# Kernel optimization log

Measured on AMD Instinct MI355X. Metric: run time of the kernel, lower is better.

## Reference

```python
import jax, jax.numpy as jnp
import numpy as np
import math

Z, N = 4, 128
EMB, L0, MLPH, GEO = 16, 32, 64, 64
NB, NH = 32, 128
C = MLPH + GEO
BETA, MAXR = 5.0, 10.0
Y0 = 0.5 / math.sqrt(math.pi)  # spherical harmonic l=0


def setup_inputs() -> dict:
    key = jax.random.key(0)
    ks = jax.random.split(key, 24)
    g = lambda i, s: jax.random.normal(ks[i], s, jnp.float32)
    inp = {}
    inp['features'] = jax.random.randint(ks[0], (Z, N, 1), 0, 6)
    inp['geometry'] = g(1, (Z, N, 3))
    inp['mask'] = jnp.ones((Z, N), jnp.float32)
    emb = g(2, (6, EMB))
    inp['emb'] = emb.at[5].set(0.0)  # padding_idx=5
    # radial MLP weights per conv layer (basis->h->h->mul_out*mul_in)
    inp['r0w0'] = g(3, (NB, NH)); inp['r0w1'] = g(4, (NH, NH)); inp['r0w2'] = g(5, (NH, L0 * EMB))
    inp['r1w0'] = g(6, (NB, NH)); inp['r1w1'] = g(7, (NH, NH)); inp['r1w2'] = g(8, (NH, L0 * L0))
    inp['r2w0'] = g(9, (NB, NH)); inp['r2w1'] = g(10, (NH, NH)); inp['r2w2'] = g(11, (NH, MLPH * L0))
    # ResnetPointnet (3 -> GEO per atom, two residual FC blocks)
    inp['pn_w0'] = g(12, (3, GEO)) * 0.3; inp['pn_b0'] = jnp.zeros((GEO,), jnp.float32)
    inp['pn_w1a'] = g(13, (GEO, GEO)) * 0.1; inp['pn_b1a'] = jnp.zeros((GEO,), jnp.float32)
    inp['pn_w1b'] = g(14, (GEO, GEO)) * 0.1; inp['pn_b1b'] = jnp.zeros((GEO,), jnp.float32)
    inp['pn_w2a'] = g(15, (GEO, GEO)) * 0.1; inp['pn_b2a'] = jnp.zeros((GEO,), jnp.float32)
    inp['pn_w2b'] = g(16, (GEO, GEO)) * 0.1; inp['pn_b2b'] = jnp.zeros((GEO,), jnp.float32)
    # output MLP + per-atom BatchNorm1d(natoms) params
    inp['e1_w'] = g(17, (C, C)) * 0.05; inp['e1_b'] = jnp.zeros((C,), jnp.float32)
    inp['bn1_g'] = jnp.ones((N,), jnp.float32); inp['bn1_b'] = jnp.zeros((N,), jnp.float32)
    inp['e2_w'] = g(18, (C, 2 * C)) * 0.05; inp['e2_b'] = jnp.zeros((2 * C,), jnp.float32)
    inp['bn2_g'] = jnp.ones((N,), jnp.float32); inp['bn2_b'] = jnp.zeros((N,), jnp.float32)
    return inp


def _sp(x):
    return jax.nn.softplus(BETA * x) / BETA


def _ssp(x):
    return _sp(x) - math.log(2.0) / BETA


def _leaky(x):
    return jnp.where(x > 0, x, 0.2 * x)


def _radial(radii, w0, w1, w2):
    # CosineBasisModel: smooth cosine^2 bumps then small MLP (e3nn-style /sqrt(fan_in))
    centers = jnp.linspace(0.0, MAXR, NB)
    step = centers[1] - centers[0]
    x = (radii[..., None] - centers) / step
    basis = jnp.where(jnp.abs(x) < 1.0, jnp.cos(0.5 * jnp.pi * x) ** 2, 0.0)  # [z,a,b,NB]
    h = _ssp(basis @ w0 / math.sqrt(NB))
    h = _ssp(h @ w1 / math.sqrt(NH))
    return h @ w2 / math.sqrt(NH)  # [z,a,b,dout*din]


def _bn(x, gamma, beta):
    # torch BatchNorm1d(natoms) on [Z, natoms, C]: normalize over (Z, C) per atom slot
    mu = jnp.mean(x, axis=(0, 2), keepdims=True)
    var = jnp.var(x, axis=(0, 2), keepdims=True)
    xn = (x - mu) * jax.lax.rsqrt(var + 1e-5)
    return xn * gamma[None, :, None] + beta[None, :, None]


def reference(features, geometry, mask, emb,
              r0w0, r0w1, r0w2, r1w0, r1w1, r1w2, r2w0, r2w1, r2w2,
              pn_w0, pn_b0, pn_w1a, pn_b1a, pn_w1b, pn_b1b,
              pn_w2a, pn_b2a, pn_w2b, pn_b2b,
              e1_w, e1_b, bn1_g, bn1_b, e2_w, e2_b, bn2_g, bn2_b):
    # constants(): pairwise geometry, detached in the original
    diff = jax.lax.stop_gradient(geometry[:, None, :, :] - geometry[:, :, None, :])  # [z,a,b,3]
    radii = jnp.linalg.norm(diff, axis=-1)  # [z,a,b]

    # ResnetPointnet: per-atom geometric features
    net = geometry @ pn_w0 + pn_b0
    for (wa, ba, wb, bb) in ((pn_w1a, pn_b1a, pn_w1b, pn_b1b), (pn_w2a, pn_b2a, pn_w2b, pn_b2b)):
        dx = jax.nn.relu(net) @ wa + ba
        dx = jax.nn.relu(dx) @ wb + bb
        net = net + dx
    geo_pn = net * mask[..., None]  # [z,n,GEO]

    # embedding
    f = emb[features[..., 0]]  # [z,n,EMB]

    # equivariant kernel-conv layers; all reps are l=0 so Y = Y0 constant
    dims = ((EMB, L0, r0w0, r0w1, r0w2), (L0, L0, r1w0, r1w1, r1w2), (L0, MLPH, r2w0, r2w1, r2w2))
    for (din, dout, w0, w1, w2) in dims:
        f = f / math.sqrt(N)
        K = _radial(radii, w0, w1, w2).reshape(Z, N, N, dout, din)
        f = jnp.einsum('zabij,zbj,zb->zai', K, f, mask) * Y0
        f = _sp(f)               # GatedBlock with all-scalar Rs -> scalar act only
        f = f * mask[..., None]

    feat = jnp.concatenate([f, geo_pn], axis=2)  # [z,n,C]
    x = _leaky(_bn(feat @ e1_w + e1_b, bn1_g, bn1_b))
    x = _leaky(_bn(x @ e2_w + e2_b, bn2_g, bn2_b))
    out = jnp.sum(x * mask[..., None], axis=1)  # Aggregate(axis=1, sum)
    return out  # [Z, 2*C]
```

## Files before the change

### kernel.cpp

```cpp
#include <hip/hip_runtime.h>
#include <math.h>

#define Zc   4
#define Nc   128
#define EMBc 16
#define L0c  32
#define MLPHc 64
#define GEOc 64
#define NBc  32
#define NHc  128
#define Cc   128
#define SLc  64

typedef float  f32x4  __attribute__((ext_vector_type(4)));
typedef short  bf16x8 __attribute__((ext_vector_type(8)));

union FragU {
    bf16x8 v;
    unsigned short u[8];
    uint2 q2[2];
};

struct P {
    const float *geom, *mask, *emb;
    const int*   features;
    const float *pw0,*pb0,*w1a,*b1a,*w1b,*b1b,*w2a,*b2a,*w2b,*b2b;
    const float *r00,*r01,*r02, *r10,*r11,*r12, *r20,*r21,*r22;
    const float *e1w,*e1b,*bn1g,*bn1b,*e2w,*e2b,*bn2g,*bn2b;
    unsigned short *h2buf, *gt, *packs;
    float *part, *f0, *geo_pn, *outp;
};

__device__ __forceinline__ float sp5(float x){
    float y = 5.0f * x;
    float t = fabsf(y);
    return (fmaxf(y, 0.0f) + log1pf(__expf(-t))) * 0.2f;
}
__device__ __forceinline__ float ssp5_post(float y){
    float e = __expf(-fabsf(y));
    float u = fmaxf(y, 0.0f) + __logf(1.0f + e);
    return fmaf(0.2f, u, -0.13862943611198906f);
}
__device__ __forceinline__ unsigned int cvtpk_bf16(float a, float b){
    unsigned int r;
    asm("v_cvt_pk_bf16_f32 %0, %1, %2" : "=v"(r) : "v"(a), "v"(b));
    return r;
}
__device__ __forceinline__ unsigned short f2bf(float f){
    unsigned int u = __float_as_uint(f);
    unsigned int r = (u + 0x7FFFu + ((u >> 16) & 1u)) >> 16;
    return (unsigned short)r;
}
__device__ __forceinline__ int kmap(int l, int e){
    return 4*((l >> 4) & 3) + (e & 3) + 16*(e >> 2);
}

__device__ void init_dev(int bx, const P& p, char* smem)
{
    float* cur = (float*)smem;
    float* tmp = cur + 4*GEOc;
    int t = threadIdx.x;
    if (bx < 128){
        int g  = t >> 6;
        int c  = t & 63;
        int zn = bx*4 + g;
        float gx = p.geom[zn*3+0], gy = p.geom[zn*3+1], gz = p.geom[zn*3+2];
        float v = fmaf(gx, p.pw0[0*GEOc+c], fmaf(gy, p.pw0[1*GEOc+c],
                  fmaf(gz, p.pw0[2*GEOc+c], p.pb0[c])));
        const float* WA[2] = {p.w1a, p.w2a}; const float* BA[2] = {p.b1a, p.b2a};
        const float* WB[2] = {p.w1b, p.w2b}; const float* BB[2] = {p.b1b, p.b2b};
        #pragma unroll
        for (int blk = 0; blk < 2; blk++){
            cur[g*GEOc + c] = v;
            __syncthreads();
            float s = BA[blk][c];
            for (int k = 0; k < GEOc; k++)
                s = fmaf(fmaxf(cur[g*GEOc + k], 0.0f), WA[blk][k*GEOc+c], s);
            tmp[g*GEOc + c] = s;
            __syncthreads();
            float s2 = BB[blk][c];
            for (int k = 0; k < GEOc; k++)
                s2 = fmaf(fmaxf(tmp[g*GEOc + k], 0.0f), WB[blk][k*GEOc+c], s2);
            v = v + s2;
            __syncthreads();
        }
        p.geo_pn[zn*GEOc + c] = v * p.mask[zn];
        if (c < EMBc){
            int fi = p.features[zn];
            p.f0[zn*EMBc + c] = p.emb[fi*EMBc + c] * p.mask[zn] * 0.0022038655607334227f;
        }
    } else if (bx < 368){
        int j = bx - 128;
        int layer = j / 80;
        int sub = j % 80;
        const float* w0s = (layer == 0) ? p.r00 : (layer == 1) ? p.r10 : p.r20;
        const float* w1s = (layer == 0) ? p.r01 : (layer == 1) ? p.r11 : p.r21;
        unsigned short* p0 = p.packs + layer*4096;
        unsigned short* p1 = p.packs + 12288 + layer*16384;
        int idx = sub*256 + t;
        if (idx < 4096){
            int t8 = idx >> 9, l = (idx >> 3) & 63, e = idx & 7;
            int k = kmap(l, e);
            int n = (t8 << 4) + (l & 15);
            p0[idx] = f2bf(w0s[k*NHc + n] * 0.8838834764831844f);
        } else {
            int jj = idx - 4096;
            int fid = jj >> 9, l = (jj >> 3) & 63, e = jj & 7;
            int kk = fid >> 3, t8 = fid & 7;
            int k = 32*kk + kmap(l, e);
            int n = 16*t8 + (l & 15);
            p1[jj] = f2bf(w1s[k*NHc + n] * 0.4419417382415922f);
        }
    } else {
        for (int i = t; i < Zc*2*Cc; i += 256) p.outp[i] = 0.0f;
    }
}

__device__ void pairmlp_dev(int vb, const P& p, char* smem)
{
    char* lb = smem;
    int t   = threadIdx.x;
    int w   = t >> 6;
    int l   = t & 63;
    int g16 = l >> 4;
    int c   = l & 15;
    int layer = vb >> 10;
    int p0  = (vb & 1023) * 64;
    int z   = p0 >> 14;
    int a   = (p0 >> 7) & 127;
    int b0  = p0 & 127;

    if (b0 + 16*w + 15 < a) return;

    const unsigned short* wp0 = p.packs + layer*4096;
    const unsigned short* wp1 = p.packs + 12288 + layer*16384;
    unsigned short* h2 = p.h2buf + (size_t)layer * ((size_t)Zc*Nc*Nc*NHc);

    int bp = b0 + 16*w + c;
    float ax = p.geom[(z*Nc + a)*3 + 0];
    float ay = p.geom[(z*Nc + a)*3 + 1];
    float az = p.geom[(z*Nc + a)*3 + 2];
    float dx = p.geom[(z*Nc + bp)*3 + 0] - ax;
    float dy = p.geom[(z*Nc + bp)*3 + 1] - ay;
    float dz = p.geom[(z*Nc + bp)*3 + 2] - az;
    float rm = sqrtf(dx*dx + dy*dy + dz*dz);

    FragU af;
    #pragma unroll
    for (int e = 0; e < 8; e++){
        int k = kmap(l, e);
        float x = fmaf(rm, 3.1f, -(float)k);
        float v = 0.0f;
        if (fabsf(x) < 1.0f){ float cc = __cosf(1.57079632679f*x); v = cc*cc; }
        af.u[e] = (unsigned short)cvtpk_bf16(v, v);
    }

    f32x4 acc[8];
    #pragma unroll
    for (int t8 = 0; t8 < 8; t8++) acc[t8] = (f32x4){0.f,0.f,0.f,0.f};
    #pragma unroll
    for (int t8 = 0; t8 < 8; t8++){
        bf16x8 bf = *reinterpret_cast<const bf16x8*>(wp0 + ((t8*64 + l) << 3));
        acc[t8] = __builtin_amdgcn_mfma_f32_16x16x32_bf16(af.v, bf, acc[t8], 0, 0, 0);
    }
    #pragma unroll
    for (int t8 = 0; t8 < 8; t8++){
        #pragma unroll
        for (int rg = 0; rg < 4; rg++){
            int m = 16*w + 4*g16 + rg;
            int n = 16*t8 + c;
            int off = ((m << 8) + (n << 1)) ^ ((m & 7) << 4);
            *(unsigned short*)(lb + off) = (unsigned short)cvtpk_bf16(ssp5_post(acc[t8][rg]), 0.0f);
        }
    }

    f32x4 acc2[8];
    #pragma unroll
    for (int t8 = 0; t8 < 8; t8++) acc2[t8] = (f32x4){0.f,0.f,0.f,0.f};
    int mrow = 16*w + c;
    int sw   = (mrow & 7) << 4;
    #pragma unroll
    for (int kk = 0; kk < 4; kk++){
        int ob = (mrow << 8) + (kk << 6) + (g16 << 3);
        FragU a2;
        a2.q2[0] = *(const uint2*)(lb + (ob ^ sw));
        a2.q2[1] = *(const uint2*)(lb + ((ob + 32) ^ sw));
        #pragma unroll
        for (int t8 = 0; t8 < 8; t8++){
            bf16x8 bf = *reinterpret_cast<const bf16x8*>(wp1 + (((kk*8 + t8)*64 + l) << 3));
            acc2[t8] = __builtin_amdgcn_mfma_f32_16x16x32_bf16(a2.v, bf, acc2[t8], 0, 0, 0);
        }
    }
    size_t zbase = (size_t)z*Nc*Nc*NHc;
    #pragma unroll
    for (int t8 = 0; t8 < 8; t8++){
        #pragma unroll
        for (int rg = 0; rg < 4; rg++){
            int m = 16*w + 4*g16 + rg;
            int b = b0 + m;
            unsigned short val = (unsigned short)cvtpk_bf16(ssp5_post(acc2[t8][rg]), 0.0f);
            h2[zbase + ((size_t)a*Nc + b)*NHc + 16*t8 + c] = val;
        }
    }
}

template<int DIN, int DOUT>
__device__ void gmat_dev(int vb, const float* f, const float* w2,
                         unsigned short* gt, char* smem)
{
    float (*fsh)[DIN] = (float (*)[DIN])smem;
    int t  = threadIdx.x;
    int bx = vb & 63, by = vb >> 6;
    int zb0 = bx * 8;
    if (t < 8*DIN){
        int r = t / DIN, j = t % DIN;
        fsh[r][j] = f[(zb0 + r)*DIN + j];
    }
    __syncthreads();
    int mi = by * 256 + t;
    int m_ = mi & (NHc-1);
    int i_ = mi >> 7;
    const float* wrow = w2 + (size_t)(m_*DOUT + i_) * DIN;
    float s[8];
    #pragma unroll
    for (int r = 0; r < 8; r++) s[r] = 0.0f;
    #pragma unroll
    for (int j4 = 0; j4 < DIN/4; j4++){
        float4 wv4 = *reinterpret_cast<const float4*>(&wrow[j4*4]);
        #pragma unroll
        for (int q = 0; q < 4; q++){
            float wv = reinterpret_cast<const float*>(&wv4)[q];
            int j = j4*4 + q;
            #pragma unroll
            for (int r = 0; r < 8; r++)
                s[r] = fmaf(fsh[r][j], wv, s[r]);
        }
    }
    int z = zb0 >> 7;
    #pragma unroll
    for (int r = 0; r < 8; r++){
        int b = (zb0 + r) & (Nc-1);
        gt[((size_t)z*DOUT + i_)*(Nc*NHc) + b*NHc + m_] = (unsigned short)cvtpk_bf16(s[r], s[r]);
    }
}

template<int DIN, int DOUT>
__device__ void egmat_dev(int vb, const float* part, const float* mask,
                          const float* w2, unsigned short* gt, char* smem)
{
    float (*fsh)[DIN] = (float (*)[DIN])smem;
    int t  = threadIdx.x;
    int bx = vb & 63, by = vb >> 6;
    int zb0 = bx * 8;
    for (int idx = t; idx < 8*DIN; idx += 256){
        int r = idx / DIN, j = idx % DIN;
        int zb = zb0 + r;
        float s = 0.0f;
        #pragma unroll
        for (int sl = 0; sl < SLc; sl++)
            s += part[(size_t)sl*(Zc*Nc*DIN) + zb*DIN + j];
        float m = mask[zb];
        fsh[r][j] = sp5(s) * m * m * 0.0022038655607334227f;
    }
    __syncthreads();
    int mi = by * 256 + t;
    int m_ = mi & (NHc-1);
    int i_ = mi >> 7;
    const float* wrow = w2 + (size_t)(m_*DOUT + i_) * DIN;
    float s[8];
    #pragma unroll
    for (int r = 0; r < 8; r++) s[r] = 0.0f;
    #pragma unroll
    for (int j4 = 0; j4 < DIN/4; j4++){
        float4 wv4 = *reinterpret_cast<const float4*>(&wrow[j4*4]);
        #pragma unroll
        for (int q = 0; q < 4; q++){
            float wv = reinterpret_cast<const float*>(&wv4)[q];
            int j = j4*4 + q;
            #pragma unroll
            for (int r = 0; r < 8; r++)
                s[r] = fmaf(fsh[r][j], wv, s[r]);
        }
    }
    int z = zb0 >> 7;
    #pragma unroll
    for (int r = 0; r < 8; r++){
        int b = (zb0 + r) & (Nc-1);
        gt[((size_t)z*DOUT + i_)*(Nc*NHc) + b*NHc + m_] = (unsigned short)cvtpk_bf16(s[r], s[r]);
    }
}

template<int DOUT, int KS>
__device__ void gemm3_dev(int vb, const unsigned short* h2, const unsigned short* gt,
                          float* partial, char* smem)
{
    constexpr int NS   = (Nc*NHc)/KS;
    constexpr int ROWB = KS*2;
    unsigned short* Ash = (unsigned short*)smem;
    unsigned short* Bsh = (unsigned short*)(smem + 64*ROWB);
    int t = threadIdx.x;
    int w = t >> 6, l = t & 63;
    int g16 = l >> 4, c16 = l & 15;
    int s  = vb % NS;
    int at = (vb / NS) & 1;
    int z  = vb / (NS*2);
    int a0 = at*64;
    int k0 = s*KS;

    {
        constexpr int ITA = (64*(KS/8))/256;
        #pragma unroll
        for (int it = 0; it < ITA; it++){
            int idx = it*256 + t;
            int r = idx / (KS/8), c8 = idx % (KS/8);
            int aRow = a0 + r;
            int kk = k0 + c8*8;
            int b  = kk >> 7;
            int m8 = kk & (NHc-1);
            const unsigned short* srcp = (b >= aRow)
                ? h2 + ((size_t)(z*Nc + aRow))*(Nc*NHc) + b*NHc + m8
                : h2 + ((size_t)(z*Nc + b))*(Nc*NHc) + aRow*NHc + m8;
            uint4 v = *reinterpret_cast<const uint4*>(srcp);
            int byte = (r*ROWB + c8*16) ^ ((r & 7) << 4);
            *reinterpret_cast<uint4*>((char*)Ash + byte) = v;
        }
    }
    {
        const unsigned short* src = gt + ((size_t)z*DOUT)*(Nc*NHc) + k0;
        constexpr int ITB = (DOUT*(KS/8))/256;
        #pragma unroll
        for (int it = 0; it < ITB; it++){
            int idx = it*256 + t;
            int r = idx / (KS/8), c8 = idx % (KS/8);
            uint4 v = *reinterpret_cast<const uint4*>(src + (size_t)r*(Nc*NHc) + c8*8);
            int byte = (r*ROWB + c8*16) ^ ((r & 7) << 4);
            *reinterpret_cast<uint4*>((char*)Bsh + byte) = v;
        }
    }
    __syncthreads();

    constexpr int NT = DOUT/16;
    f32x4 acc[NT];
    #pragma unroll
    for (int nt = 0; nt < NT; nt++) acc[nt] = (f32x4){0.f,0.f,0.f,0.f};
    int ar  = 16*w + c16;
    int asw = (ar & 7) << 4;
    #pragma unroll
    for (int ks = 0; ks < KS/32; ks++){
        FragU afr;
        int abyte = ar*ROWB + ks*64 + g16*8;
        afr.q2[0] = *(const uint2*)((char*)Ash + (abyte ^ asw));
        afr.q2[1] = *(const uint2*)((char*)Ash + ((abyte + 32) ^ asw));
        #pragma unroll
        for (int nt = 0; nt < NT; nt++){
            int br  = nt*16 + c16;
            int bsw = (br & 7) << 4;
            int bbyte = br*ROWB + ks*64 + g16*8;
            FragU bfr;
            bfr.q2[0] = *(const uint2*)((char*)Bsh + (bbyte ^ bsw));
            bfr.q2[1] = *(const uint2*)((char*)Bsh + ((bbyte + 32) ^ bsw));
            acc[nt] = __builtin_amdgcn_mfma_f32_16x16x32_bf16(afr.v, bfr.v, acc[nt], 0, 0, 0);
        }
    }
    #pragma unroll
    for (int nt = 0; nt < NT; nt++){
        #pragma unroll
        for (int rg = 0; rg < 4; rg++){
            int a = a0 + 16*w + 4*g16 + rg;
            int i = nt*16 + c16;
            partial[(((size_t)s*Zc + z)*Nc + a)*DOUT + i] = acc[nt][rg];
        }
    }
}

__device__ void tail_dev(int n, const P& p, char* smem)
{
    float* feat = (float*)smem;
    float* xln  = feat + Zc*Cc;
    float* r1   = xln + Zc*Cc;
    float* r2   = r1 + 4;
    int t = threadIdx.x;

    {
        int z = t >> 6, i = t & 63;
        float s = 0.0f;
        #pragma unroll
        for (int sl = 0; sl < SLc; sl++)
            s += p.part[((size_t)sl*Zc*Nc + z*Nc + n)*MLPHc + i];
        float m = p.mask[z*Nc + n];
        feat[z*Cc + i] = sp5(s) * m;
        feat[z*Cc + MLPHc + i] = p.geo_pn[(z*Nc + n)*GEOc + i];
    }
    __syncthreads();

    int c  = t & 127;
    int zh = t >> 7;
    float x1v[2];
    float sum = 0.0f, sq = 0.0f;
    #pragma unroll
    for (int q = 0; q < 2; q++){
        int z = zh*2 + q;
        float s = p.e1b[c];
        for (int k = 0; k < Cc; k++) s = fmaf(feat[z*Cc + k], p.e1w[k*Cc + c], s);
        x1v[q] = s; sum += s; sq = fmaf(s, s, sq);
    }
    #pragma unroll
    for (int off = 32; off > 0; off >>= 1){
        sum += __shfl_down(sum, off);
        sq  += __shfl_down(sq,  off);
    }
    if ((t & 63) == 0){ r1[t >> 6] = sum; r2[t >> 6] = sq; }
    __syncthreads();
    {
        float tot  = r1[0]+r1[1]+r1[2]+r1[3];
        float totq = r2[0]+r2[1]+r2[2]+r2[3];
        float mu   = tot * (1.0f/512.0f);
        float var  = totq * (1.0f/512.0f) - mu*mu;
        float rstd = rsqrtf(var + 1e-5f);
        float ga = p.bn1g[n], be = p.bn1b[n];
        #pragma unroll
        for (int q = 0; q < 2; q++){
            float v = (x1v[q] - mu) * rstd * ga + be;
            xln[(zh*2 + q)*Cc + c] = v > 0.0f ? v : 0.2f*v;
        }
    }
    __syncthreads();

    float x2v[4];
    sum = 0.0f; sq = 0.0f;
    #pragma unroll
    for (int z = 0; z < Zc; z++){
        float s = p.e2b[t];
        for (int k = 0; k < Cc; k++) s = fmaf(xln[z*Cc + k], p.e2w[k*2*Cc + t], s);
        x2v[z] = s; sum += s; sq = fmaf(s, s, sq);
    }
    #pragma unroll
    for (int off = 32; off > 0; off >>= 1){
        sum += __shfl_down(sum, off);
        sq  += __shfl_down(sq,  off);
    }
    if ((t & 63) == 0){ r1[t >> 6] = sum; r2[t >> 6] = sq; }
    __syncthreads();
    {
        float tot  = r1[0]+r1[1]+r1[2]+r1[3];
        float totq = r2[0]+r2[1]+r2[2]+r2[3];
        float mu   = tot * (1.0f/1024.0f);
        float var  = totq * (1.0f/1024.0f) - mu*mu;
        float rstd = rsqrtf(var + 1e-5f);
        float ga = p.bn2g[n], be = p.bn2b[n];
        #pragma unroll
        for (int z = 0; z < Zc; z++){
            float v = (x2v[z] - mu) * rstd * ga + be;
            v = v > 0.0f ? v : 0.2f*v;
            atomicAdd(&p.outp[z*2*Cc + t], v * p.mask[z*Nc + n]);
        }
    }
}

__global__ __launch_bounds__(256) void k_init_g(P p){
    __shared__ __align__(16) char smem[2048];
    init_dev(blockIdx.x, p, smem);
}
__global__ __launch_bounds__(256, 2) void k_pg(P p){
    __shared__ __align__(16) char smem[16384];
    int bx = blockIdx.x;
    if (bx < 3072){
        pairmlp_dev(bx, p, smem);
    } else {
        gmat_dev<16,32>(bx - 3072, p.f0, p.r02, p.gt, smem);
    }
}
template<int DIN, int DOUT>
__global__ __launch_bounds__(256) void k_egmat_g(P p, const float* w2){
    __shared__ __align__(16) char smem[8*DIN*4];
    egmat_dev<DIN,DOUT>(blockIdx.y*64 + blockIdx.x, p.part, p.mask, w2, p.gt, smem);
}
template<int DOUT, int KS>
__global__ __launch_bounds__(256) void k_gemm3_g(P p, const unsigned short* h2){
    __shared__ __align__(16) char smem[(64+DOUT)*KS*2];
    constexpr int NS = (Nc*NHc)/KS;
    int vb = (blockIdx.z*2 + blockIdx.y)*NS + blockIdx.x;
    gemm3_dev<DOUT,KS>(vb, h2, p.gt, p.part, smem);
}
__global__ __launch_bounds__(256) void k_tail_g(P p){
    __shared__ __align__(16) char smem[4224];
    tail_dev(blockIdx.x, p, smem);
}

extern "C" void kernel_launch(void* const* d_in, const int* in_sizes, int n_in,
                              void* d_out, int out_size, void* d_ws, size_t ws_size,
                              hipStream_t stream)
{
    P p;
    p.features = (const int*)  d_in[0];
    p.geom     = (const float*)d_in[1];
    p.mask     = (const float*)d_in[2];
    p.emb      = (const float*)d_in[3];
    p.r00 = (const float*)d_in[4];  p.r01 = (const float*)d_in[5];  p.r02 = (const float*)d_in[6];
    p.r10 = (const float*)d_in[7];  p.r11 = (const float*)d_in[8];  p.r12 = (const float*)d_in[9];
    p.r20 = (const float*)d_in[10]; p.r21 = (const float*)d_in[11]; p.r22 = (const float*)d_in[12];
    p.pw0 = (const float*)d_in[13]; p.pb0 = (const float*)d_in[14];
    p.w1a = (const float*)d_in[15]; p.b1a = (const float*)d_in[16];
    p.w1b = (const float*)d_in[17]; p.b1b = (const float*)d_in[18];
    p.w2a = (const float*)d_in[19]; p.b2a = (const float*)d_in[20];
    p.w2b = (const float*)d_in[21]; p.b2b = (const float*)d_in[22];
    p.e1w = (const float*)d_in[23]; p.e1b = (const float*)d_in[24];
    p.bn1g= (const float*)d_in[25]; p.bn1b= (const float*)d_in[26];
    p.e2w = (const float*)d_in[27]; p.e2b = (const float*)d_in[28];
    p.bn2g= (const float*)d_in[29]; p.bn2b= (const float*)d_in[30];

    float* ws = (float*)d_ws;
    p.h2buf = (unsigned short*)ws;
    p.gt    = (unsigned short*)(ws + 12582912);
    p.part  = ws + 12582912 + 2097152;
    p.f0    = p.part + 2097152;
    p.geo_pn= p.f0 + 8192;
    p.packs = (unsigned short*)(p.geo_pn + 32768);
    p.outp  = (float*)d_out;
    (void)ws_size; (void)in_sizes; (void)n_in; (void)out_size;

    const size_t H2L = (size_t)Zc*Nc*Nc*NHc;

    k_init_g<<<369, 256, 0, stream>>>(p);
    k_pg<<<4096, 256, 0, stream>>>(p);
    k_gemm3_g<32,256><<<dim3(64, 2, Zc), 256, 0, stream>>>(p, p.h2buf);
    k_egmat_g<32,32><<<dim3(64, 16), 256, 0, stream>>>(p, p.r12);
    k_gemm3_g<32,256><<<dim3(64, 2, Zc), 256, 0, stream>>>(p, p.h2buf + H2L);
    k_egmat_g<32,64><<<dim3(64, 32), 256, 0, stream>>>(p, p.r22);
    k_gemm3_g<64,256><<<dim3(64, 2, Zc), 256, 0, stream>>>(p, p.h2buf + 2*H2L);
    k_tail_g<<<128, 256, 0, stream>>>(p);
}
```

Measured before the change: 154.4 us.

## Split pair MLP into single-wave blocks over only needed triangular tiles

The fused pair-MLP/gmat kernel now launches 64-thread blocks, one wavefront per 16-pair tile, in place of 256-thread blocks holding four waves. Block indices map directly onto the triangular set of (a, b-chunk) tiles that are actually needed, so no launched waves exit early when their tile lies below the diagonal. The gmat part is re-tiled for 64 threads. This removes idle or early-exit waves and the load imbalance inside blocks. In exchange it launches more blocks, adds a sqrt-based index decode per block, and gives up the 2-blocks-per-CU launch bound.

```diff
diff --git a/kernel.cpp b/kernel.cpp
--- a/kernel.cpp
+++ b/kernel.cpp
@@ -116,27 +116,18 @@
     }
 }
 
-__device__ void pairmlp_dev(int vb, const P& p, char* smem)
+__device__ void pairmlp_dev(int layer, int z, int a, int bc, const P& p, char* smem)
 {
     char* lb = smem;
-    int t   = threadIdx.x;
-    int w   = t >> 6;
-    int l   = t & 63;
+    int l   = threadIdx.x;
     int g16 = l >> 4;
     int c   = l & 15;
-    int layer = vb >> 10;
-    int p0  = (vb & 1023) * 64;
-    int z   = p0 >> 14;
-    int a   = (p0 >> 7) & 127;
-    int b0  = p0 & 127;
-
-    if (b0 + 16*w + 15 < a) return;
 
     const unsigned short* wp0 = p.packs + layer*4096;
     const unsigned short* wp1 = p.packs + 12288 + layer*16384;
     unsigned short* h2 = p.h2buf + (size_t)layer * ((size_t)Zc*Nc*Nc*NHc);
 
-    int bp = b0 + 16*w + c;
+    int bp = bc + c;
     float ax = p.geom[(z*Nc + a)*3 + 0];
     float ay = p.geom[(z*Nc + a)*3 + 1];
     float az = p.geom[(z*Nc + a)*3 + 2];
@@ -167,17 +158,18 @@
     for (int t8 = 0; t8 < 8; t8++){
         #pragma unroll
         for (int rg = 0; rg < 4; rg++){
-            int m = 16*w + 4*g16 + rg;
+            int m = 4*g16 + rg;
             int n = 16*t8 + c;
             int off = ((m << 8) + (n << 1)) ^ ((m & 7) << 4);
             *(unsigned short*)(lb + off) = (unsigned short)cvtpk_bf16(ssp5_post(acc[t8][rg]), 0.0f);
         }
     }
+    __syncthreads();
 
     f32x4 acc2[8];
     #pragma unroll
     for (int t8 = 0; t8 < 8; t8++) acc2[t8] = (f32x4){0.f,0.f,0.f,0.f};
-    int mrow = 16*w + c;
+    int mrow = c;
     int sw   = (mrow & 7) << 4;
     #pragma unroll
     for (int kk = 0; kk < 4; kk++){
@@ -196,36 +188,40 @@
     for (int t8 = 0; t8 < 8; t8++){
         #pragma unroll
         for (int rg = 0; rg < 4; rg++){
-            int m = 16*w + 4*g16 + rg;
-            int b = b0 + m;
+            int m = 4*g16 + rg;
+            int b = bc + m;
             unsigned short val = (unsigned short)cvtpk_bf16(ssp5_post(acc2[t8][rg]), 0.0f);
             h2[zbase + ((size_t)a*Nc + b)*NHc + 16*t8 + c] = val;
         }
     }
 }
 
-template<int DIN, int DOUT>
-__device__ void gmat_dev(int vb, const float* f, const float* w2,
-                         unsigned short* gt, char* smem)
-{
-    float (*fsh)[DIN] = (float (*)[DIN])smem;
+__device__ void gmat64_dev(int vb, const float* f, const float* w2,
+                           unsigned short* gt, char* smem)
+{
+    float (*fsh)[EMBc] = (float (*)[EMBc])smem;
     int t  = threadIdx.x;
-    int bx = vb & 63, by = vb >> 6;
-    int zb0 = bx * 8;
-    if (t < 8*DIN){
-        int r = t / DIN, j = t % DIN;
-        fsh[r][j] = f[(zb0 + r)*DIN + j];
-    }
-    __syncthreads();
-    int mi = by * 256 + t;
+    int gbx = vb >> 6;
+    int msub = vb & 63;
+    int zb0 = gbx * 8;
+    {
+        int idx = t;
+        #pragma unroll
+        for (int q = 0; q < 2; q++, idx += 64){
+            int r = idx >> 4, j = idx & 15;
+            fsh[r][j] = f[(zb0 + r)*EMBc + j];
+        }
+    }
+    __syncthreads();
+    int mi = msub*64 + t;
     int m_ = mi & (NHc-1);
     int i_ = mi >> 7;
-    const float* wrow = w2 + (size_t)(m_*DOUT + i_) * DIN;
+    const float* wrow = w2 + (size_t)(m_*L0c + i_) * EMBc;
     float s[8];
     #pragma unroll
     for (int r = 0; r < 8; r++) s[r] = 0.0f;
     #pragma unroll
-    for (int j4 = 0; j4 < DIN/4; j4++){
+    for (int j4 = 0; j4 < EMBc/4; j4++){
         float4 wv4 = *reinterpret_cast<const float4*>(&wrow[j4*4]);
         #pragma unroll
         for (int q = 0; q < 4; q++){
@@ -240,7 +236,7 @@
     #pragma unroll
     for (int r = 0; r < 8; r++){
         int b = (zb0 + r) & (Nc-1);
-        gt[((size_t)z*DOUT + i_)*(Nc*NHc) + b*NHc + m_] = (unsigned short)cvtpk_bf16(s[r], s[r]);
+        gt[((size_t)z*L0c + i_)*(Nc*NHc) + b*NHc + m_] = (unsigned short)cvtpk_bf16(s[r], s[r]);
     }
 }
 
@@ -461,13 +457,22 @@
     __shared__ __align__(16) char smem[2048];
     init_dev(blockIdx.x, p, smem);
 }
-__global__ __launch_bounds__(256, 2) void k_pg(P p){
-    __shared__ __align__(16) char smem[16384];
+__global__ __launch_bounds__(64) void k_pm(P p){
+    __shared__ __align__(16) char smem[4096];
     int bx = blockIdx.x;
-    if (bx < 3072){
-        pairmlp_dev(bx, p, smem);
+    if (bx < 6912){
+        int layer = bx / 2304;
+        int rem   = bx - layer*2304;
+        int z     = rem / 576;
+        int u     = rem - z*576;
+        int k = (int)((sqrtf(2.0f*(float)u + 4.0f) - 2.0f) * 0.25f);
+        while (8*(k+1)*(k+2) <= u) ++k;
+        while (k > 0 && 8*k*(k+1) > u) --k;
+        int a  = u - 8*k*(k+1);
+        int bc = 16*k;
+        pairmlp_dev(layer, z, a, bc, p, smem);
     } else {
-        gmat_dev<16,32>(bx - 3072, p.f0, p.r02, p.gt, smem);
+        gmat64_dev(bx - 6912, p.f0, p.r02, p.gt, smem);
     }
 }
 template<int DIN, int DOUT>
@@ -522,7 +527,7 @@
     const size_t H2L = (size_t)Zc*Nc*Nc*NHc;
 
     k_init_g<<<369, 256, 0, stream>>>(p);
-    k_pg<<<4096, 256, 0, stream>>>(p);
+    k_pm<<<11008, 64, 0, stream>>>(p);
     k_gemm3_g<32,256><<<dim3(64, 2, Zc), 256, 0, stream>>>(p, p.h2buf);
     k_egmat_g<32,32><<<dim3(64, 16), 256, 0, stream>>>(p, p.r12);
     k_gemm3_g<32,256><<<dim3(64, 2, Zc), 256, 0, stream>>>(p, p.h2buf + H2L);
```

Result: faster. 146.2 us (median of 2 runs) (-5.3%).
